# Kernel optimization log

Measured on AMD Instinct MI355X. Metric: run time of the kernel, lower is better.

## Reference

```python
import jax, jax.numpy as jnp
import numpy as np

B, NQ, NK = 8, 16384, 16384
FEAT, MID, CTX, OUT = 128, 16, 128, 128
EPS = 1e-5


def setup_inputs() -> dict:
    key = jax.random.key(0)
    ks = jax.random.split(key, 7)
    s_in = 1.0 / np.sqrt(FEAT)
    s_ctx = 1.0 / np.sqrt(CTX)
    return {
        "feature": jax.random.normal(ks[0], (B, NQ, FEAT), dtype=jnp.float32),
        "context": jax.random.normal(ks[1], (B, NK, CTX), dtype=jnp.float32),
        "Wq": jax.random.uniform(ks[2], (FEAT, MID), jnp.float32, -s_in, s_in),
        "Wk": jax.random.uniform(ks[3], (CTX, MID), jnp.float32, -s_ctx, s_ctx),
        "Wv": jax.random.uniform(ks[4], (CTX, OUT), jnp.float32, -s_ctx, s_ctx),
        "gamma": jnp.ones((MID,), jnp.float32),
        "beta": jnp.zeros((MID,), jnp.float32),
    }


def reference(feature, context, Wq, Wk, Wv, gamma, beta):
    # per-token linear projections (QKVTransformV2 with heads=1)
    query = feature @ Wq                     # [B, Nq, mid]
    key = context @ Wk                       # [B, Nk, mid]
    value = context @ Wv                     # [B, Nk, out]
    # softmax over context positions (dim=1)
    sm = jax.nn.softmax(key, axis=1)         # [B, Nk, mid]
    # content lambda: softmax^T @ value -> [B, mid, out]
    lam = jnp.einsum("bnm,bnd->bmd", sm, value)
    # BatchNorm1d(mid) in training mode: stats over (batch, length=out)
    mean = jnp.mean(lam, axis=(0, 2), keepdims=True)
    var = jnp.var(lam, axis=(0, 2), keepdims=True)  # biased, matches torch BN
    bn = (lam - mean) * jax.lax.rsqrt(var + EPS)
    bn = bn * gamma[None, :, None] + beta[None, :, None]
    # final query matmul -> [B, Nq, out]
    return jnp.einsum("bqm,bmd->bqd", query, bn)
```

## Files before the change

### kernel.cpp

```cpp
#include <hip/hip_runtime.h>
#include <cstddef>

#define BATCH 8
#define NQ 16384
#define NK 16384
#define FEAT 128
#define MID 16
#define CTXD 128
#define OUTD 128
#define EPSV 1e-5f

#define ROWS 256


__global__ __launch_bounds__(256) void k_phase1(
    const float* __restrict__ ctx, const float* __restrict__ Wk,
    float* __restrict__ U, float* __restrict__ sumw)
{
    const int b  = blockIdx.y;
    const int r0 = blockIdx.x * ROWS;
    const int t  = threadIdx.x;
    __shared__ float wL[ROWS][MID];

    {
        const int r = r0 + t;
        const float4* cp = (const float4*)(ctx + ((size_t)b * NK + r) * CTXD);
        float key[MID];
        #pragma unroll
        for (int m = 0; m < MID; ++m) key[m] = 0.f;
        #pragma unroll 4
        for (int kc = 0; kc < CTXD / 4; ++kc) {
            float4 c4 = cp[kc];
            float cf[4] = {c4.x, c4.y, c4.z, c4.w};
            #pragma unroll
            for (int j = 0; j < 4; ++j) {
                #pragma unroll
                for (int m = 0; m < MID; ++m)
                    key[m] += cf[j] * Wk[(4 * kc + j) * MID + m];
            }
        }
        #pragma unroll
        for (int m = 0; m < MID; ++m) wL[t][m] = __expf(key[m]);
    }
    __syncthreads();

    const int d = t & 127;
    const int h = t >> 7;
    float acc[MID];
    #pragma unroll
    for (int m = 0; m < MID; ++m) acc[m] = 0.f;
    for (int n = h; n < ROWS; n += 2) {
        float c = ctx[((size_t)b * NK + r0 + n) * CTXD + d];
        const float4* wp = (const float4*)wL[n];
        float4 ww[4] = {wp[0], wp[1], wp[2], wp[3]};
        const float* wf = (const float*)ww;
        #pragma unroll
        for (int m = 0; m < MID; ++m) acc[m] += wf[m] * c;
    }
    if (t < MID) {
        float s = 0.f;
        for (int n = 0; n < ROWS; ++n) s += wL[n][t];
        atomicAdd(&sumw[b * MID + t], s);
    }
    __syncthreads();
    if (h == 1) {
        #pragma unroll
        for (int m = 0; m < MID; ++m) wL[d][m] = acc[m];
    }
    __syncthreads();
    if (h == 0) {
        #pragma unroll
        for (int m = 0; m < MID; ++m)
            atomicAdd(&U[((size_t)b * MID + m) * CTXD + d], acc[m] + wL[d][m]);
    }
}

__global__ __launch_bounds__(256) void k_lam(
    const float* __restrict__ U, const float* __restrict__ sumw,
    const float* __restrict__ Wv, float* __restrict__ lam, float* __restrict__ st)
{
    const int b = blockIdx.y;
    const int e = blockIdx.x * 256 + threadIdx.x;
    const int m = e >> 7;
    const int d = e & 127;
    const float* u = U + ((size_t)b * MID + m) * CTXD;
    float dot = 0.f;
    #pragma unroll 8
    for (int k = 0; k < CTXD; ++k)
        dot += u[k] * Wv[k * OUTD + d];
    float l = dot / sumw[b * MID + m];
    lam[((size_t)b * MID + m) * OUTD + d] = l;
    float s1 = l, s2 = l * l;
    #pragma unroll
    for (int off = 32; off > 0; off >>= 1) {
        s1 += __shfl_down(s1, off);
        s2 += __shfl_down(s2, off);
    }
    if ((threadIdx.x & 63) == 0) {
        atomicAdd(&st[m], s1);
        atomicAdd(&st[MID + m], s2);
    }
}

__global__ __launch_bounds__(256) void k_out(
    const float* __restrict__ feat, const float* __restrict__ Wq,
    const float* __restrict__ lam, const float* __restrict__ st,
    const float* __restrict__ gamma, const float* __restrict__ beta,
    float* __restrict__ out)
{
    const int b  = blockIdx.y;
    const int r0 = blockIdx.x * ROWS;
    const int t  = threadIdx.x;
    __shared__ float bnL[MID][OUTD];
    __shared__ float qL[ROWS][MID];

    for (int e = t; e < MID * OUTD; e += 256) {
        int m = e >> 7, d = e & 127;
        float mean = st[m] * (1.f / (BATCH * OUTD));
        float var  = st[MID + m] * (1.f / (BATCH * OUTD)) - mean * mean;
        float inv  = rsqrtf(var + EPSV);
        bnL[m][d] = (lam[((size_t)b * MID + m) * OUTD + d] - mean) * inv * gamma[m] + beta[m];
    }

    {
        const int r = r0 + t;
        const float4* fp = (const float4*)(feat + ((size_t)b * NQ + r) * FEAT);
        float q[MID];
        #pragma unroll
        for (int m = 0; m < MID; ++m) q[m] = 0.f;
        #pragma unroll 4
        for (int kc = 0; kc < FEAT / 4; ++kc) {
            float4 f4 = fp[kc];
            float ff[4] = {f4.x, f4.y, f4.z, f4.w};
            #pragma unroll
            for (int j = 0; j < 4; ++j) {
                #pragma unroll
                for (int m = 0; m < MID; ++m)
                    q[m] += ff[j] * Wq[(4 * kc + j) * MID + m];
            }
        }
        #pragma unroll
        for (int m = 0; m < MID; ++m) qL[t][m] = q[m];
    }
    __syncthreads();

    const int d = t & 127;
    const int h = t >> 7;
    float bnr[MID];
    #pragma unroll
    for (int m = 0; m < MID; ++m) bnr[m] = bnL[m][d];
    for (int n = h; n < ROWS; n += 2) {
        const float4* qp = (const float4*)qL[n];
        float4 qq[4] = {qp[0], qp[1], qp[2], qp[3]};
        const float* qf = (const float*)qq;
        float o = 0.f;
        #pragma unroll
        for (int m = 0; m < MID; ++m) o += qf[m] * bnr[m];
        out[((size_t)b * NQ + r0 + n) * OUTD + d] = o;
    }
}

extern "C" void kernel_launch(void* const* d_in, const int* in_sizes, int n_in,
                              void* d_out, int out_size, void* d_ws, size_t ws_size,
                              hipStream_t stream)
{
    const float* feat  = (const float*)d_in[0];
    const float* ctx   = (const float*)d_in[1];
    const float* Wq    = (const float*)d_in[2];
    const float* Wk    = (const float*)d_in[3];
    const float* Wv    = (const float*)d_in[4];
    const float* gamma = (const float*)d_in[5];
    const float* beta  = (const float*)d_in[6];
    float* out = (float*)d_out;

    float* ws   = (float*)d_ws;
    float* U    = ws;
    float* sumw = ws + 16384;
    float* st   = ws + 16512;
    float* lam  = ws + 16544;

    hipMemsetAsync(d_ws, 0, 16544 * sizeof(float), stream);
    k_phase1<<<dim3(NK / ROWS, BATCH), 256, 0, stream>>>(ctx, Wk, U, sumw);
    k_lam<<<dim3(8, BATCH), 256, 0, stream>>>(U, sumw, Wv, lam, st);
    k_out<<<dim3(NQ / ROWS, BATCH), 256, 0, stream>>>(feat, Wq, lam, st, gamma, beta, out);
}
```

Measured before the change: 258.4 us.

## Stage row tiles in LDS and split projection work across wavefronts

Both the key-projection kernel and the output kernel now copy a 64-row tile into padded shared memory with coalesced float4 loads. Each wavefront computes 4 of the 16 projection columns per row, so each lane holds fewer accumulators. Phase 1 broadcasts exp weights with readlane instead of going through LDS. The output kernel uses a register-blocked 4-row by 8-column outer product with float4 stores. The goal is to drop uncoalesced per-thread row reads and shared-memory traffic, at the cost of four times more blocks and more atomics into U and sumw.

```diff
diff --git a/kernel.cpp b/kernel.cpp
--- a/kernel.cpp
+++ b/kernel.cpp
@@ -10,68 +10,97 @@
 #define OUTD 128
 #define EPSV 1e-5f
 
-#define ROWS 256
-
+#define ROWS 64
+#define LPAD 132
+
+
+__device__ __forceinline__ float readlane_f(float v, int lane) {
+    return __uint_as_float(__builtin_amdgcn_readlane(__float_as_uint(v), lane));
+}
 
 __global__ __launch_bounds__(256) void k_phase1(
     const float* __restrict__ ctx, const float* __restrict__ Wk,
     float* __restrict__ U, float* __restrict__ sumw)
 {
+    __shared__ float cL[ROWS * LPAD];
     const int b  = blockIdx.y;
     const int r0 = blockIdx.x * ROWS;
     const int t  = threadIdx.x;
-    __shared__ float wL[ROWS][MID];
-
-    {
-        const int r = r0 + t;
-        const float4* cp = (const float4*)(ctx + ((size_t)b * NK + r) * CTXD);
-        float key[MID];
-        #pragma unroll
-        for (int m = 0; m < MID; ++m) key[m] = 0.f;
-        #pragma unroll 4
-        for (int kc = 0; kc < CTXD / 4; ++kc) {
-            float4 c4 = cp[kc];
-            float cf[4] = {c4.x, c4.y, c4.z, c4.w};
-            #pragma unroll
-            for (int j = 0; j < 4; ++j) {
-                #pragma unroll
-                for (int m = 0; m < MID; ++m)
-                    key[m] += cf[j] * Wk[(4 * kc + j) * MID + m];
-            }
-        }
-        #pragma unroll
-        for (int m = 0; m < MID; ++m) wL[t][m] = __expf(key[m]);
+    const int lane = t & 63;
+
+    {
+        const float4* g4 = (const float4*)(ctx + ((size_t)b * NK + r0) * CTXD);
+        float4* c4p = (float4*)cL;
+        #pragma unroll
+        for (int i = 0; i < 8; ++i) {
+            int idx = t + 256 * i;
+            int row = idx >> 5;
+            int c4  = idx & 31;
+            c4p[row * (LPAD / 4) + c4] = g4[idx];
+        }
     }
     __syncthreads();
 
-    const int d = t & 127;
-    const int h = t >> 7;
-    float acc[MID];
-    #pragma unroll
-    for (int m = 0; m < MID; ++m) acc[m] = 0.f;
-    for (int n = h; n < ROWS; n += 2) {
-        float c = ctx[((size_t)b * NK + r0 + n) * CTXD + d];
-        const float4* wp = (const float4*)wL[n];
-        float4 ww[4] = {wp[0], wp[1], wp[2], wp[3]};
-        const float* wf = (const float*)ww;
-        #pragma unroll
-        for (int m = 0; m < MID; ++m) acc[m] += wf[m] * c;
-    }
-    if (t < MID) {
-        float s = 0.f;
-        for (int n = 0; n < ROWS; ++n) s += wL[n][t];
-        atomicAdd(&sumw[b * MID + t], s);
-    }
-    __syncthreads();
-    if (h == 1) {
-        #pragma unroll
-        for (int m = 0; m < MID; ++m) wL[d][m] = acc[m];
-    }
-    __syncthreads();
-    if (h == 0) {
-        #pragma unroll
-        for (int m = 0; m < MID; ++m)
-            atomicAdd(&U[((size_t)b * MID + m) * CTXD + d], acc[m] + wL[d][m]);
+    const int g = __builtin_amdgcn_readfirstlane(t >> 6);
+    float k0 = 0.f, k1 = 0.f, k2 = 0.f, k3 = 0.f;
+    {
+        const float4* cr = (const float4*)cL + lane * (LPAD / 4);
+        const float* wkb = Wk + 4 * g;
+        #pragma unroll 8
+        for (int kq = 0; kq < 32; ++kq) {
+            float4 c4 = cr[kq];
+            const float* w0p = wkb + (4 * kq + 0) * MID;
+            const float* w1p = wkb + (4 * kq + 1) * MID;
+            const float* w2p = wkb + (4 * kq + 2) * MID;
+            const float* w3p = wkb + (4 * kq + 3) * MID;
+            k0 += c4.x * w0p[0]; k1 += c4.x * w0p[1]; k2 += c4.x * w0p[2]; k3 += c4.x * w0p[3];
+            k0 += c4.y * w1p[0]; k1 += c4.y * w1p[1]; k2 += c4.y * w1p[2]; k3 += c4.y * w1p[3];
+            k0 += c4.z * w2p[0]; k1 += c4.z * w2p[1]; k2 += c4.z * w2p[2]; k3 += c4.z * w2p[3];
+            k0 += c4.w * w3p[0]; k1 += c4.w * w3p[1]; k2 += c4.w * w3p[2]; k3 += c4.w * w3p[3];
+        }
+    }
+    float w0 = __expf(k0), w1 = __expf(k1), w2 = __expf(k2), w3 = __expf(k3);
+
+    {
+        float s0 = w0, s1 = w1, s2 = w2, s3 = w3;
+        #pragma unroll
+        for (int off = 32; off > 0; off >>= 1) {
+            s0 += __shfl_xor(s0, off);
+            s1 += __shfl_xor(s1, off);
+            s2 += __shfl_xor(s2, off);
+            s3 += __shfl_xor(s3, off);
+        }
+        if (lane == 0) {
+            atomicAdd(&sumw[b * MID + 4 * g + 0], s0);
+            atomicAdd(&sumw[b * MID + 4 * g + 1], s1);
+            atomicAdd(&sumw[b * MID + 4 * g + 2], s2);
+            atomicAdd(&sumw[b * MID + 4 * g + 3], s3);
+        }
+    }
+
+    float a00 = 0.f, a01 = 0.f, a10 = 0.f, a11 = 0.f;
+    float a20 = 0.f, a21 = 0.f, a30 = 0.f, a31 = 0.f;
+    #pragma unroll 4
+    for (int n2 = 0; n2 < ROWS; ++n2) {
+        float b0 = readlane_f(w0, n2);
+        float b1 = readlane_f(w1, n2);
+        float b2 = readlane_f(w2, n2);
+        float b3 = readlane_f(w3, n2);
+        float2 c2 = *(const float2*)(cL + n2 * LPAD + 2 * lane);
+        a00 += b0 * c2.x; a01 += b0 * c2.y;
+        a10 += b1 * c2.x; a11 += b1 * c2.y;
+        a20 += b2 * c2.x; a21 += b2 * c2.y;
+        a30 += b3 * c2.x; a31 += b3 * c2.y;
+    }
+    {
+        float* u0 = U + ((size_t)b * MID + 4 * g + 0) * CTXD + 2 * lane;
+        float* u1 = U + ((size_t)b * MID + 4 * g + 1) * CTXD + 2 * lane;
+        float* u2 = U + ((size_t)b * MID + 4 * g + 2) * CTXD + 2 * lane;
+        float* u3 = U + ((size_t)b * MID + 4 * g + 3) * CTXD + 2 * lane;
+        atomicAdd(u0, a00); atomicAdd(u0 + 1, a01);
+        atomicAdd(u1, a10); atomicAdd(u1 + 1, a11);
+        atomicAdd(u2, a20); atomicAdd(u2 + 1, a21);
+        atomicAdd(u3, a30); atomicAdd(u3 + 1, a31);
     }
 }
 
@@ -108,55 +137,98 @@
     const float* __restrict__ gamma, const float* __restrict__ beta,
     float* __restrict__ out)
 {
+    __shared__ float fL[ROWS * LPAD];
+    __shared__ float qL[ROWS * 20];
+    __shared__ float bnL[MID * LPAD];
     const int b  = blockIdx.y;
     const int r0 = blockIdx.x * ROWS;
     const int t  = threadIdx.x;
-    __shared__ float bnL[MID][OUTD];
-    __shared__ float qL[ROWS][MID];
-
-    for (int e = t; e < MID * OUTD; e += 256) {
+    const int lane = t & 63;
+
+    #pragma unroll
+    for (int i = 0; i < 8; ++i) {
+        int e = t + 256 * i;
         int m = e >> 7, d = e & 127;
         float mean = st[m] * (1.f / (BATCH * OUTD));
         float var  = st[MID + m] * (1.f / (BATCH * OUTD)) - mean * mean;
         float inv  = rsqrtf(var + EPSV);
-        bnL[m][d] = (lam[((size_t)b * MID + m) * OUTD + d] - mean) * inv * gamma[m] + beta[m];
-    }
-
-    {
-        const int r = r0 + t;
-        const float4* fp = (const float4*)(feat + ((size_t)b * NQ + r) * FEAT);
-        float q[MID];
-        #pragma unroll
-        for (int m = 0; m < MID; ++m) q[m] = 0.f;
-        #pragma unroll 4
-        for (int kc = 0; kc < FEAT / 4; ++kc) {
-            float4 f4 = fp[kc];
-            float ff[4] = {f4.x, f4.y, f4.z, f4.w};
+        bnL[m * LPAD + d] =
+            (lam[((size_t)b * MID + m) * OUTD + d] - mean) * inv * gamma[m] + beta[m];
+    }
+    {
+        const float4* g4 = (const float4*)(feat + ((size_t)b * NQ + r0) * FEAT);
+        float4* f4p = (float4*)fL;
+        #pragma unroll
+        for (int i = 0; i < 8; ++i) {
+            int idx = t + 256 * i;
+            int row = idx >> 5;
+            int c4  = idx & 31;
+            f4p[row * (LPAD / 4) + c4] = g4[idx];
+        }
+    }
+    __syncthreads();
+
+    {
+        const int g = __builtin_amdgcn_readfirstlane(t >> 6);
+        float q0 = 0.f, q1 = 0.f, q2 = 0.f, q3 = 0.f;
+        const float4* fr = (const float4*)fL + lane * (LPAD / 4);
+        const float* wqb = Wq + 4 * g;
+        #pragma unroll 8
+        for (int kq = 0; kq < 32; ++kq) {
+            float4 c4 = fr[kq];
+            const float* w0p = wqb + (4 * kq + 0) * MID;
+            const float* w1p = wqb + (4 * kq + 1) * MID;
+            const float* w2p = wqb + (4 * kq + 2) * MID;
+            const float* w3p = wqb + (4 * kq + 3) * MID;
+            q0 += c4.x * w0p[0]; q1 += c4.x * w0p[1]; q2 += c4.x * w0p[2]; q3 += c4.x * w0p[3];
+            q0 += c4.y * w1p[0]; q1 += c4.y * w1p[1]; q2 += c4.y * w1p[2]; q3 += c4.y * w1p[3];
+            q0 += c4.z * w2p[0]; q1 += c4.z * w2p[1]; q2 += c4.z * w2p[2]; q3 += c4.z * w2p[3];
+            q0 += c4.w * w3p[0]; q1 += c4.w * w3p[1]; q2 += c4.w * w3p[2]; q3 += c4.w * w3p[3];
+        }
+        ((float4*)qL)[lane * 5 + g] = make_float4(q0, q1, q2, q3);
+    }
+    __syncthreads();
+
+    {
+        const int nblk = t >> 4;
+        const int dq   = t & 15;
+        const float4* qL4  = (const float4*)qL;
+        const float4* bnL4 = (const float4*)bnL;
+        float qv[4][16];
+        #pragma unroll
+        for (int rr = 0; rr < 4; ++rr) {
             #pragma unroll
-            for (int j = 0; j < 4; ++j) {
-                #pragma unroll
-                for (int m = 0; m < MID; ++m)
-                    q[m] += ff[j] * Wq[(4 * kc + j) * MID + m];
+            for (int mq = 0; mq < 4; ++mq) {
+                float4 v = qL4[(4 * nblk + rr) * 5 + mq];
+                qv[rr][4 * mq + 0] = v.x; qv[rr][4 * mq + 1] = v.y;
+                qv[rr][4 * mq + 2] = v.z; qv[rr][4 * mq + 3] = v.w;
             }
         }
-        #pragma unroll
-        for (int m = 0; m < MID; ++m) qL[t][m] = q[m];
-    }
-    __syncthreads();
-
-    const int d = t & 127;
-    const int h = t >> 7;
-    float bnr[MID];
-    #pragma unroll
-    for (int m = 0; m < MID; ++m) bnr[m] = bnL[m][d];
-    for (int n = h; n < ROWS; n += 2) {
-        const float4* qp = (const float4*)qL[n];
-        float4 qq[4] = {qp[0], qp[1], qp[2], qp[3]};
-        const float* qf = (const float*)qq;
-        float o = 0.f;
-        #pragma unroll
-        for (int m = 0; m < MID; ++m) o += qf[m] * bnr[m];
-        out[((size_t)b * NQ + r0 + n) * OUTD + d] = o;
+        float acc[4][8];
+        #pragma unroll
+        for (int rr = 0; rr < 4; ++rr)
+            #pragma unroll
+            for (int j = 0; j < 8; ++j) acc[rr][j] = 0.f;
+
+        #pragma unroll
+        for (int m = 0; m < 16; ++m) {
+            float4 b0 = bnL4[m * (LPAD / 4) + 2 * dq];
+            float4 b1 = bnL4[m * (LPAD / 4) + 2 * dq + 1];
+            #pragma unroll
+            for (int rr = 0; rr < 4; ++rr) {
+                float qq = qv[rr][m];
+                acc[rr][0] += qq * b0.x; acc[rr][1] += qq * b0.y;
+                acc[rr][2] += qq * b0.z; acc[rr][3] += qq * b0.w;
+                acc[rr][4] += qq * b1.x; acc[rr][5] += qq * b1.y;
+                acc[rr][6] += qq * b1.z; acc[rr][7] += qq * b1.w;
+            }
+        }
+        #pragma unroll
+        for (int rr = 0; rr < 4; ++rr) {
+            float4* op = (float4*)(out + ((size_t)b * NQ + r0 + 4 * nblk + rr) * OUTD + 8 * dq);
+            op[0] = make_float4(acc[rr][0], acc[rr][1], acc[rr][2], acc[rr][3]);
+            op[1] = make_float4(acc[rr][4], acc[rr][5], acc[rr][6], acc[rr][7]);
+        }
     }
 }
 
```

Result: slower. 407.7 us (+57.8%).
